# Performance work log

Measured on AMD Instinct MI355X. Metric: run time of the kernel, lower is better.

Reference implementation:

```python
import jax, jax.numpy as jnp
import numpy as np

NUM_USER = 10000
NUM_ITEM = 30000
N = NUM_USER + NUM_ITEM          # total nodes
DIM = 64                          # dim_E == dim_C
E = 500000                        # user-item interactions
NUM_ROUTING = 3
ALPHA_THR = 0.5
NEG_SLOPE_ATTN = 0.2              # GAT attention leaky slope
NEG_SLOPE_ACT = 0.01              # F.leaky_relu_ default


def l2norm(x, eps=1e-12):
    n = jnp.linalg.norm(x, axis=-1, keepdims=True)
    return x / jnp.maximum(n, eps)


def seg_softmax(score, seg):
    # numerically-stable softmax over edges grouped by destination node
    m = jax.ops.segment_max(score, seg, num_segments=N)
    e = jnp.exp(score - m[seg])
    s = jax.ops.segment_sum(e, seg, num_segments=N)
    return e / (s[seg] + 1e-16)


def gat_ori(x, W, src, dst):
    # GATConv_ori: dot-product attention, softmax per destination, scatter-add
    h = x @ W                                     # [N, C]
    score = jax.nn.leaky_relu(jnp.sum(h[dst] * h[src], -1), NEG_SLOPE_ATTN)
    alpha = seg_softmax(score, dst)               # [2E]
    return jax.ops.segment_sum(alpha[:, None] * h[src], dst, num_segments=N)


def gat_pre(x, y, z, W, src, dst):
    # GATConv_pre: primary-modality attention modulated by cross-modal gate (reattn)
    hx = x @ W
    sx = jnp.sum(hx[dst] * hx[src], -1)
    sy = jnp.sum(y[dst] * y[src], -1)
    sz = jnp.sum(z[dst] * z[src], -1)
    alpha = seg_softmax(jax.nn.leaky_relu(sx, NEG_SLOPE_ATTN), dst)
    gate = jax.nn.sigmoid(0.5 * (sy + sz))
    alpha = jnp.where(gate > ALPHA_THR, alpha * gate, alpha)
    return jax.ops.segment_sum(alpha[:, None] * hx[src], dst, num_segments=N)


def cgcn(pref, feat, pref2, feat2, pref3, feat3, src, dst, Wpre, Wori):
    x = jnp.concatenate([pref, feat], 0)
    y = jnp.concatenate([pref2, feat2], 0)
    z = jnp.concatenate([pref3, feat3], 0)
    x = l2norm(gat_pre(x, y, z, Wpre, src, dst))
    for _ in range(NUM_ROUTING):
        x = l2norm(x + gat_ori(x, Wori, src, dst))
    return x


def gcn_conv(x, W, src, dst):
    return jax.ops.segment_sum((x @ W)[src], dst, num_segments=N)


def real_gcn(id_emb, Wg, src, dst):
    x = l2norm(id_emb)
    h1 = jax.nn.leaky_relu(gcn_conv(x, Wg[0], src, dst), NEG_SLOPE_ACT)
    h2 = jax.nn.leaky_relu(gcn_conv(h1, Wg[1], src, dst), NEG_SLOPE_ACT)
    h3 = gcn_conv(h1, Wg[2], src, dst)
    return x + h1 + h2 + h3


def setup_inputs() -> dict:
    key = jax.random.key(0)
    ks = jax.random.split(key, 16)
    users = jax.random.randint(ks[0], (E,), 0, NUM_USER)
    items = jax.random.randint(ks[1], (E,), NUM_USER, N)
    edge_index = jnp.stack([users, items]).astype(jnp.int64)
    s = 0.05
    return {
        'edge_index': edge_index,
        'v_feat': jax.random.normal(ks[2], (NUM_ITEM, 128), jnp.float32),
        'a_feat': jax.random.normal(ks[3], (NUM_ITEM, 128), jnp.float32),
        't_feat': jax.random.normal(ks[4], (NUM_ITEM, 100), jnp.float32),
        'pref_v': jax.random.normal(ks[5], (NUM_USER, DIM), jnp.float32) * s,
        'pref_a': jax.random.normal(ks[6], (NUM_USER, DIM), jnp.float32) * s,
        'pref_t': jax.random.normal(ks[7], (NUM_USER, DIM), jnp.float32) * s,
        'mlp_v_w': jax.random.normal(ks[8], (DIM, 128), jnp.float32) * s,
        'mlp_v_b': jnp.zeros((DIM,), jnp.float32),
        'mlp_a_w': jax.random.normal(ks[9], (DIM, 128), jnp.float32) * s,
        'mlp_a_b': jnp.zeros((DIM,), jnp.float32),
        'mlp_t_w': jax.random.normal(ks[10], (DIM, 100), jnp.float32) * s,
        'mlp_t_b': jnp.zeros((DIM,), jnp.float32),
        'pre_w': jax.random.normal(ks[11], (3, DIM, DIM), jnp.float32) * s,
        'ori_w': jax.random.normal(ks[12], (3, DIM, DIM), jnp.float32) * s,
        'gcn_w': jax.random.normal(ks[13], (3, DIM, DIM), jnp.float32) * s,
        'id_embedding': jax.random.normal(ks[14], (N, DIM), jnp.float32) * s,
    }


def reference(edge_index, v_feat, a_feat, t_feat, pref_v, pref_a, pref_t,
              mlp_v_w, mlp_v_b, mlp_a_w, mlp_a_b, mlp_t_w, mlp_t_b,
              pre_w, ori_w, gcn_w, id_embedding):
    # symmetrize edges (cat with flipped); no self-loops possible (bipartite)
    src = jnp.concatenate([edge_index[0], edge_index[1]])
    dst = jnp.concatenate([edge_index[1], edge_index[0]])

    fv = l2norm(jax.nn.leaky_relu(v_feat @ mlp_v_w.T + mlp_v_b, NEG_SLOPE_ACT))
    fa = l2norm(jax.nn.leaky_relu(a_feat @ mlp_a_w.T + mlp_a_b, NEG_SLOPE_ACT))
    ft = l2norm(jax.nn.leaky_relu(t_feat @ mlp_t_w.T + mlp_t_b, NEG_SLOPE_ACT))
    pv, pa, pt = l2norm(pref_v), l2norm(pref_a), l2norm(pref_t)

    v_rep = cgcn(pv, fv, pa, fa, pt, ft, src, dst, pre_w[0], ori_w[0])
    a_rep = cgcn(pa, fa, pv, fv, pt, ft, src, dst, pre_w[1], ori_w[1])
    t_rep = cgcn(pt, ft, pa, fa, pv, fv, src, dst, pre_w[2], ori_w[2])
    id_rep = real_gcn(id_embedding, gcn_w, src, dst)

    return jnp.concatenate([id_rep, v_rep, a_rep, t_rep], axis=1)  # [N, 4*DIM]
```

## Files before the change

kernel.cpp:

```cpp
#include <hip/hip_runtime.h>
#include <hip/hip_fp16.h>
#include <math.h>

#define NUSER 10000
#define NITEM 30000
#define NN    40000
#define DD    64
#define PLANE ((size_t)NN * DD)

typedef _Float16 hv2 __attribute__((ext_vector_type(2)));
typedef _Float16 half8v __attribute__((ext_vector_type(8)));
typedef float float4v __attribute__((ext_vector_type(4)));
union U2H { unsigned u; hv2 v; __half2 hh; };

#if defined(__has_builtin)
#if __has_builtin(__builtin_amdgcn_fdot2)
#define HAS_FDOT2 1
#endif
#endif

__device__ __forceinline__ float fdot2u(unsigned a, unsigned b, float c) {
#ifdef HAS_FDOT2
    U2H x, y;
    x.u = a;
    y.u = b;
    return __builtin_amdgcn_fdot2(x.v, y.v, c, false);
#else
    U2H x, y;
    x.u = a;
    y.u = b;
    float2 fa = __half22float2(x.hh), fb = __half22float2(y.hh);
    return c + fa.x * fb.x + fa.y * fb.y;
#endif
}

__device__ __forceinline__ float dot8(uint4 a, uint4 b) {
    float d = fdot2u(a.x, b.x, 0.f);
    d = fdot2u(a.y, b.y, d);
    d = fdot2u(a.z, b.z, d);
    d = fdot2u(a.w, b.w, d);
    return d;
}

__device__ __forceinline__ __half2 uh(unsigned u) { U2H x; x.u = u; return x.hh; }
__device__ __forceinline__ unsigned hu(__half2 h) { U2H x; x.hh = h; return x.u; }
__device__ __forceinline__ __half2 h2rx(__half2 v, int m) {
    return __hadd2(v, uh((unsigned)__shfl_xor((int)hu(v), m, 64)));
}

__device__ __forceinline__ float wsum(float v) {
#pragma unroll
    for (int o = 32; o > 0; o >>= 1) v += __shfl_xor(v, o, 64);
    return v;
}
__device__ __forceinline__ float qsum8(float v) {
    v += __shfl_xor(v, 1, 64);
    v += __shfl_xor(v, 2, 64);
    v += __shfl_xor(v, 4, 64);
    return v;
}
__device__ __forceinline__ float gsum8(float v) {
    v += __shfl_xor(v, 8, 64);
    v += __shfl_xor(v, 16, 64);
    v += __shfl_xor(v, 32, 64);
    return v;
}

__device__ __forceinline__ int nodeperm(int i) {
    return ((i & 3) == 0) ? (i >> 2) : (NUSER + i - 1 - (i >> 2));
}

__global__ void k_hist(const int* ei, int E2, int E, int* cnt, int* posw) {
    int i = blockIdx.x * blockDim.x + threadIdx.x;
    if (i >= E2) return;
    int d = (i < E) ? ei[E + i] : ei[i - E];
    posw[i] = atomicAdd(&cnt[d], 1);
}

__global__ void k_bsum(const int* __restrict__ cnt, int* __restrict__ bsum, int n, int chunk) {
    __shared__ int wsh[4];
    int b = blockIdx.x, tid = threadIdx.x;
    int base = b * chunk, end = min(n, base + chunk);
    int s = 0;
    for (int i = base + tid; i < end; i += 256) s += cnt[i];
#pragma unroll
    for (int o = 32; o > 0; o >>= 1) s += __shfl_xor(s, o, 64);
    if ((tid & 63) == 0) wsh[tid >> 6] = s;
    __syncthreads();
    if (tid == 0) bsum[b] = wsh[0] + wsh[1] + wsh[2] + wsh[3];
}

__global__ void k_bscan(int* bsum, int nb, int* rp_end) {
    int lane = threadIdx.x;
    int v = (lane < nb) ? bsum[lane] : 0;
    int orig = v;
#pragma unroll
    for (int o = 1; o < 64; o <<= 1) {
        int y = __shfl_up(v, o, 64);
        if (lane >= o) v += y;
    }
    if (lane < nb) bsum[lane] = v - orig;
    if (lane == 63) *rp_end = v;
}

__global__ void k_apply(const int* __restrict__ cnt, const int* __restrict__ boff,
                        int* __restrict__ rp, int n, int chunk) {
    __shared__ int buf[256];
    __shared__ int csh;
    int b = blockIdx.x, tid = threadIdx.x;
    int base = b * chunk, end = min(n, base + chunk);
    int carry = boff[b];
    for (int t0 = base; t0 < end; t0 += 256) {
        int i = t0 + tid;
        int v = (i < end) ? cnt[i] : 0;
        int x = v;
        buf[tid] = x;
        __syncthreads();
        for (int o = 1; o < 256; o <<= 1) {
            int y = (tid >= o) ? buf[tid - o] : 0;
            __syncthreads();
            x += y;
            buf[tid] = x;
            __syncthreads();
        }
        if (i < end) rp[i] = carry + x - v;
        __syncthreads();
        if (tid == 255) csh = carry + x;
        __syncthreads();
        carry = csh;
    }
}

__global__ void k_scatter(const int* ei, int E2, int E, const int* rp,
                          const int* __restrict__ posw, int* col) {
    int i = blockIdx.x * blockDim.x + threadIdx.x;
    if (i >= E2) return;
    int j = (i < E) ? i : i - E;
    int s = (i < E) ? ei[j] : ei[E + j];
    int d = (i < E) ? ei[E + j] : ei[j];
    col[rp[d] + posw[i]] = s;
}

__global__ void k_prep_pref(const float* __restrict__ pv, const float* __restrict__ pa,
                            const float* __restrict__ pt, __half* __restrict__ M) {
    int t = blockIdx.x * blockDim.x + threadIdx.x;
    int w = t >> 6, lane = t & 63, nw = (gridDim.x * blockDim.x) >> 6;
    for (int r = w; r < NUSER; r += nw) {
        float a = pv[(size_t)r * DD + lane];
        float b = pa[(size_t)r * DD + lane];
        float c = pt[(size_t)r * DD + lane];
        float sa = a * a, sb = b * b, sc = c * c;
#pragma unroll
        for (int o = 32; o > 0; o >>= 1) {
            sa += __shfl_xor(sa, o, 64);
            sb += __shfl_xor(sb, o, 64);
            sc += __shfl_xor(sc, o, 64);
        }
        size_t base = (size_t)r * 3 * DD + lane;
        M[base] = __float2half(a / fmaxf(sqrtf(sa), 1e-12f));
        M[base + DD] = __float2half(b / fmaxf(sqrtf(sb), 1e-12f));
        M[base + 2 * DD] = __float2half(c / fmaxf(sqrtf(sc), 1e-12f));
    }
}

template <int K>
__global__ void k_mlp(const float* __restrict__ feat, const float* __restrict__ W,
                      const float* __restrict__ bias, __half* __restrict__ M, int mo) {
    constexpr int K4 = K / 4;
    __shared__ float4 Wl[K4][DD];
    __shared__ float4 rbuf[4][2][K4];
    int t = threadIdx.x, wib = t >> 6, lane = t & 63;
    for (int i = t; i < DD * K4; i += 256) {
        int c = i / K4, k4 = i - c * K4;
        Wl[k4][c] = *(const float4*)(W + (size_t)c * K + k4 * 4);
    }
    __syncthreads();
    float b = bias[lane];
    const int stride = gridDim.x * 4;
    int r = blockIdx.x * 4 + wib;
    float4 v = {0.f, 0.f, 0.f, 0.f};
    if (r < NITEM && lane < K4) v = *(const float4*)(feat + (size_t)r * K + lane * 4);
    int cur = 0;
    for (; r < NITEM; r += stride) {
        if (lane < K4) rbuf[wib][cur][lane] = v;
        int rn = r + stride;
        if (rn < NITEM && lane < K4) v = *(const float4*)(feat + (size_t)rn * K + lane * 4);
        asm volatile("s_waitcnt lgkmcnt(0)" ::: "memory");
        float acc = b;
#pragma unroll
        for (int k4 = 0; k4 < K4; k4++) {
            float4 x4 = rbuf[wib][cur][k4];
            float4 w4 = Wl[k4][lane];
            acc += x4.x * w4.x + x4.y * w4.y + x4.z * w4.z + x4.w * w4.w;
        }
        float h = acc > 0.f ? acc : 0.01f * acc;
        float n = sqrtf(wsum(h * h));
        M[((size_t)(NUSER + r) * 3 + mo) * DD + lane] = __float2half(h / fmaxf(n, 1e-12f));
        cur ^= 1;
    }
}

__global__ void k_gemm_mfma(const __half* __restrict__ x3, const float* __restrict__ W3,
                            __half* __restrict__ o3) {
    int mo = blockIdx.y;
    const float* W = W3 + (size_t)mo * 4096;
    int t = threadIdx.x, wv = t >> 6, lane = t & 63;
    int lr = lane & 15, lg = lane >> 4;
    half8v b[4][2];
#pragma unroll
    for (int ct = 0; ct < 4; ct++)
#pragma unroll
        for (int kh = 0; kh < 2; kh++)
#pragma unroll
            for (int i = 0; i < 8; i++)
                b[ct][kh][i] = (_Float16)W[(kh * 32 + lg * 8 + i) * 64 + ct * 16 + lr];
    const int NT = NN / 16;
    for (int rt = blockIdx.x * 4 + wv; rt < NT; rt += gridDim.x * 4) {
        const __half* xr = x3 + ((size_t)(rt * 16 + lr) * 3 + mo) * DD + lg * 8;
        half8v a0 = *(const half8v*)xr;
        half8v a1 = *(const half8v*)(xr + 32);
        float4v acc0 = {0.f, 0.f, 0.f, 0.f}, acc1 = acc0, acc2 = acc0, acc3 = acc0;
        acc0 = __builtin_amdgcn_mfma_f32_16x16x32_f16(a0, b[0][0], acc0, 0, 0, 0);
        acc1 = __builtin_amdgcn_mfma_f32_16x16x32_f16(a0, b[1][0], acc1, 0, 0, 0);
        acc2 = __builtin_amdgcn_mfma_f32_16x16x32_f16(a0, b[2][0], acc2, 0, 0, 0);
        acc3 = __builtin_amdgcn_mfma_f32_16x16x32_f16(a0, b[3][0], acc3, 0, 0, 0);
        acc0 = __builtin_amdgcn_mfma_f32_16x16x32_f16(a1, b[0][1], acc0, 0, 0, 0);
        acc1 = __builtin_amdgcn_mfma_f32_16x16x32_f16(a1, b[1][1], acc1, 0, 0, 0);
        acc2 = __builtin_amdgcn_mfma_f32_16x16x32_f16(a1, b[2][1], acc2, 0, 0, 0);
        acc3 = __builtin_amdgcn_mfma_f32_16x16x32_f16(a1, b[3][1], acc3, 0, 0, 0);
#pragma unroll
        for (int i = 0; i < 4; i++) {
            size_t rbase = ((size_t)(rt * 16 + lg * 4 + i) * 3 + mo) * DD + lr;
            o3[rbase] = __float2half(acc0[i]);
            o3[rbase + 16] = __float2half(acc1[i]);
            o3[rbase + 32] = __float2half(acc2[i]);
            o3[rbase + 48] = __float2half(acc3[i]);
        }
    }
}

__global__ void k_gemm_f2(const float* __restrict__ x, const float* __restrict__ W2,
                          __half* __restrict__ o2) {
    __shared__ float rowbuf[4][DD];
    int mo = blockIdx.y;
    const float* W = W2 + (size_t)mo * 4096;
    int t = threadIdx.x, wib = t >> 6, lane = t & 63;
    float Wc[DD];
#pragma unroll
    for (int k = 0; k < DD; k++) Wc[k] = W[k * DD + lane];
    for (int r = blockIdx.x * 4 + wib; r < NN; r += gridDim.x * 4) {
        rowbuf[wib][lane] = x[(size_t)r * DD + lane];
        asm volatile("s_waitcnt lgkmcnt(0)" ::: "memory");
        float acc = 0.f;
#pragma unroll
        for (int k4 = 0; k4 < DD / 4; k4++) {
            float4 xq = *(const float4*)&rowbuf[wib][k4 * 4];
            acc += xq.x * Wc[k4 * 4] + xq.y * Wc[k4 * 4 + 1] + xq.z * Wc[k4 * 4 + 2] +
                   xq.w * Wc[k4 * 4 + 3];
        }
        o2[((size_t)r * 2 + mo) * DD + lane] = __float2half(acc);
    }
}

__global__ void k_gemm_id(const float* __restrict__ x, const float* __restrict__ W,
                          __half* __restrict__ hout, float* __restrict__ xnorm) {
    __shared__ float rowbuf[4][DD];
    int t = threadIdx.x, wib = t >> 6, lane = t & 63;
    float Wc[DD];
#pragma unroll
    for (int k = 0; k < DD; k++) Wc[k] = W[k * DD + lane];
    for (int r = blockIdx.x * 4 + wib; r < NN; r += gridDim.x * 4) {
        float xv = x[(size_t)r * DD + lane];
        float n = sqrtf(wsum(xv * xv));
        xv /= fmaxf(n, 1e-12f);
        xnorm[(size_t)r * DD + lane] = xv;
        rowbuf[wib][lane] = xv;
        asm volatile("s_waitcnt lgkmcnt(0)" ::: "memory");
        float acc = 0.f;
#pragma unroll
        for (int k4 = 0; k4 < DD / 4; k4++) {
            float4 xq = *(const float4*)&rowbuf[wib][k4 * 4];
            acc += xq.x * Wc[k4 * 4] + xq.y * Wc[k4 * 4 + 1] + xq.z * Wc[k4 * 4 + 2] +
                   xq.w * Wc[k4 * 4 + 3];
        }
        hout[(size_t)r * DD + lane] = __float2half(acc);
    }
}

__device__ __forceinline__ float gatef(float ssum) {
    float gate = 1.f / (1.f + __expf(-0.5f * ssum));
    return gate > 0.5f ? gate : 1.f;
}

__global__ void k_edgedot3(const __half* __restrict__ M, const int* __restrict__ rp,
                           const int* __restrict__ col, __half* __restrict__ gf4) {
    int t = blockIdx.x * blockDim.x + threadIdx.x;
    int wv = t >> 6, lane = t & 63, nw = (gridDim.x * blockDim.x) >> 6;
    int g = lane >> 3, q = lane & 7;
    for (int w0 = wv; w0 < NN; w0 += nw) {
        int n = nodeperm(w0);
        int e0 = rp[n], e1 = rp[n + 1];
        if (e0 == e1) continue;
        const uint4* trow = (const uint4*)(M + (size_t)n * 192);
        uint4 tv = trow[q], ta = trow[q + 8], tt = trow[q + 16];
        for (int eb = e0 + g; eb < e1; eb += 8) {
            int sn = col[eb];
            const uint4* srow = (const uint4*)(M + (size_t)sn * 192);
            uint4 sv = srow[q], sa = srow[q + 8], st = srow[q + 16];
            float dv = dot8(tv, sv), da = dot8(ta, sa), dt = dot8(tt, st);
            dv = qsum8(dv);
            da = qsum8(da);
            dt = qsum8(dt);
            if (q == 0) {
                U2H p01, p2;
                p01.hh = __floats2half2_rn(gatef(da + dt), gatef(dv + dt));
                p2.hh = __floats2half2_rn(gatef(da + dv), 0.f);
                *(uint2*)(gf4 + (size_t)eb * 4) = make_uint2(p01.u, p2.u);
            }
        }
    }
}

__global__ void k_gat_pre3(const __half* __restrict__ h3, const __half* __restrict__ gf4,
                           const int* __restrict__ rp, const int* __restrict__ col,
                           __half* __restrict__ x3h) {
    int t = blockIdx.x * blockDim.x + threadIdx.x;
    int wv = t >> 6, lane = t & 63, nw = (gridDim.x * blockDim.x) >> 6;
    int g = lane >> 3, q = lane & 7;
    const __half2 z = __floats2half2_rn(0.f, 0.f);
    for (int w0 = wv; w0 < NN; w0 += nw) {
        int n = nodeperm(w0);
        int e0 = rp[n], e1 = rp[n + 1];
        const uint4* hrow = (const uint4*)(h3 + (size_t)n * 192);
        uint4 hd0 = hrow[q], hd1 = hrow[q + 8], hd2 = hrow[q + 16];
        float s0 = 0.f, s1 = 0.f, s2 = 0.f;
        __half2 a0[4] = {z, z, z, z}, a1[4] = {z, z, z, z}, a2[4] = {z, z, z, z};
        for (int eb = e0 + g; eb < e1; eb += 8) {
            int sn = col[eb];
            const uint4* srow = (const uint4*)(h3 + (size_t)sn * 192);
            uint4 v0 = srow[q], v1 = srow[q + 8], v2 = srow[q + 16];
            uint2 gv = *(const uint2*)(gf4 + (size_t)eb * 4);
            float d0 = dot8(hd0, v0), d1 = dot8(hd1, v1), d2 = dot8(hd2, v2);
            d0 = qsum8(d0);
            d1 = qsum8(d1);
            d2 = qsum8(d2);
            float2 g01 = __half22float2(uh(gv.x));
            float g2 = __half22float2(uh(gv.y)).x;
            float sc0 = d0 > 0.f ? d0 : 0.2f * d0;
            float sc1 = d1 > 0.f ? d1 : 0.2f * d1;
            float sc2 = d2 > 0.f ? d2 : 0.2f * d2;
            float p0 = __expf(sc0), p1 = __expf(sc1), p2 = __expf(sc2);
            s0 += p0;
            s1 += p1;
            s2 += p2;
            __half2 ph0 = __float2half2_rn(p0 * g01.x);
            __half2 ph1 = __float2half2_rn(p1 * g01.y);
            __half2 ph2 = __float2half2_rn(p2 * g2);
            a0[0] = __hfma2(ph0, uh(v0.x), a0[0]);
            a0[1] = __hfma2(ph0, uh(v0.y), a0[1]);
            a0[2] = __hfma2(ph0, uh(v0.z), a0[2]);
            a0[3] = __hfma2(ph0, uh(v0.w), a0[3]);
            a1[0] = __hfma2(ph1, uh(v1.x), a1[0]);
            a1[1] = __hfma2(ph1, uh(v1.y), a1[1]);
            a1[2] = __hfma2(ph1, uh(v1.z), a1[2]);
            a1[3] = __hfma2(ph1, uh(v1.w), a1[3]);
            a2[0] = __hfma2(ph2, uh(v2.x), a2[0]);
            a2[1] = __hfma2(ph2, uh(v2.y), a2[1]);
            a2[2] = __hfma2(ph2, uh(v2.z), a2[2]);
            a2[3] = __hfma2(ph2, uh(v2.w), a2[3]);
        }
        s0 = gsum8(s0);
        s1 = gsum8(s1);
        s2 = gsum8(s2);
#pragma unroll
        for (int j = 0; j < 4; j++) {
            a0[j] = h2rx(h2rx(h2rx(a0[j], 8), 16), 32);
            a1[j] = h2rx(h2rx(h2rx(a1[j], 8), 16), 32);
            a2[j] = h2rx(h2rx(h2rx(a2[j], 8), 16), 32);
        }
        float i0 = 1.f / (s0 + 1e-16f), i1 = 1.f / (s1 + 1e-16f), i2 = 1.f / (s2 + 1e-16f);
        float o0[8], o1[8], o2[8];
#pragma unroll
        for (int j = 0; j < 4; j++) {
            float2 f0 = __half22float2(a0[j]);
            float2 f1 = __half22float2(a1[j]);
            float2 f2 = __half22float2(a2[j]);
            o0[2 * j] = f0.x * i0;
            o0[2 * j + 1] = f0.y * i0;
            o1[2 * j] = f1.x * i1;
            o1[2 * j + 1] = f1.y * i1;
            o2[2 * j] = f2.x * i2;
            o2[2 * j + 1] = f2.y * i2;
        }
        float n0 = 0.f, n1 = 0.f, n2 = 0.f;
#pragma unroll
        for (int k = 0; k < 8; k++) {
            n0 += o0[k] * o0[k];
            n1 += o1[k] * o1[k];
            n2 += o2[k] * o2[k];
        }
        n0 = qsum8(n0);
        n1 = qsum8(n1);
        n2 = qsum8(n2);
        float r0 = 1.f / fmaxf(sqrtf(n0), 1e-12f);
        float r1 = 1.f / fmaxf(sqrtf(n1), 1e-12f);
        float r2 = 1.f / fmaxf(sqrtf(n2), 1e-12f);
        if (g == 0) {
            uint4* orow = (uint4*)(x3h + (size_t)n * 192);
            uint4 w0_, w1_, w2_;
            w0_.x = hu(__floats2half2_rn(o0[0] * r0, o0[1] * r0));
            w0_.y = hu(__floats2half2_rn(o0[2] * r0, o0[3] * r0));
            w0_.z = hu(__floats2half2_rn(o0[4] * r0, o0[5] * r0));
            w0_.w = hu(__floats2half2_rn(o0[6] * r0, o0[7] * r0));
            w1_.x = hu(__floats2half2_rn(o1[0] * r1, o1[1] * r1));
            w1_.y = hu(__floats2half2_rn(o1[2] * r1, o1[3] * r1));
            w1_.z = hu(__floats2half2_rn(o1[4] * r1, o1[5] * r1));
            w1_.w = hu(__floats2half2_rn(o1[6] * r1, o1[7] * r1));
            w2_.x = hu(__floats2half2_rn(o2[0] * r2, o2[1] * r2));
            w2_.y = hu(__floats2half2_rn(o2[2] * r2, o2[3] * r2));
            w2_.z = hu(__floats2half2_rn(o2[4] * r2, o2[5] * r2));
            w2_.w = hu(__floats2half2_rn(o2[6] * r2, o2[7] * r2));
            orow[q] = w0_;
            orow[q + 8] = w1_;
            orow[q + 16] = w2_;
        }
    }
}

__global__ void k_gat_ori3(const __half* __restrict__ h3, const __half* __restrict__ x3h,
                           const int* __restrict__ rp, const int* __restrict__ col,
                           __half* __restrict__ xout, float* __restrict__ fout) {
    int t = blockIdx.x * blockDim.x + threadIdx.x;
    int wv = t >> 6, lane = t & 63, nw = (gridDim.x * blockDim.x) >> 6;
    int g = lane >> 3, q = lane & 7;
    const __half2 z = __floats2half2_rn(0.f, 0.f);
    for (int w0 = wv; w0 < NN; w0 += nw) {
        int n = nodeperm(w0);
        int e0 = rp[n], e1 = rp[n + 1];
        const uint4* hrow = (const uint4*)(h3 + (size_t)n * 192);
        uint4 hd0 = hrow[q], hd1 = hrow[q + 8], hd2 = hrow[q + 16];
        float s0 = 0.f, s1 = 0.f, s2 = 0.f;
        __half2 a0[4] = {z, z, z, z}, a1[4] = {z, z, z, z}, a2[4] = {z, z, z, z};
        for (int eb = e0 + g; eb < e1; eb += 8) {
            int sn = col[eb];
            const uint4* srow = (const uint4*)(h3 + (size_t)sn * 192);
            uint4 v0 = srow[q], v1 = srow[q + 8], v2 = srow[q + 16];
            float d0 = dot8(hd0, v0), d1 = dot8(hd1, v1), d2 = dot8(hd2, v2);
            d0 = qsum8(d0);
            d1 = qsum8(d1);
            d2 = qsum8(d2);
            float sc0 = d0 > 0.f ? d0 : 0.2f * d0;
            float sc1 = d1 > 0.f ? d1 : 0.2f * d1;
            float sc2 = d2 > 0.f ? d2 : 0.2f * d2;
            float p0 = __expf(sc0), p1 = __expf(sc1), p2 = __expf(sc2);
            s0 += p0;
            s1 += p1;
            s2 += p2;
            __half2 ph0 = __float2half2_rn(p0);
            __half2 ph1 = __float2half2_rn(p1);
            __half2 ph2 = __float2half2_rn(p2);
            a0[0] = __hfma2(ph0, uh(v0.x), a0[0]);
            a0[1] = __hfma2(ph0, uh(v0.y), a0[1]);
            a0[2] = __hfma2(ph0, uh(v0.z), a0[2]);
            a0[3] = __hfma2(ph0, uh(v0.w), a0[3]);
            a1[0] = __hfma2(ph1, uh(v1.x), a1[0]);
            a1[1] = __hfma2(ph1, uh(v1.y), a1[1]);
            a1[2] = __hfma2(ph1, uh(v1.z), a1[2]);
            a1[3] = __hfma2(ph1, uh(v1.w), a1[3]);
            a2[0] = __hfma2(ph2, uh(v2.x), a2[0]);
            a2[1] = __hfma2(ph2, uh(v2.y), a2[1]);
            a2[2] = __hfma2(ph2, uh(v2.z), a2[2]);
            a2[3] = __hfma2(ph2, uh(v2.w), a2[3]);
        }
        s0 = gsum8(s0);
        s1 = gsum8(s1);
        s2 = gsum8(s2);
#pragma unroll
        for (int j = 0; j < 4; j++) {
            a0[j] = h2rx(h2rx(h2rx(a0[j], 8), 16), 32);
            a1[j] = h2rx(h2rx(h2rx(a1[j], 8), 16), 32);
            a2[j] = h2rx(h2rx(h2rx(a2[j], 8), 16), 32);
        }
        float i0 = 1.f / (s0 + 1e-16f), i1 = 1.f / (s1 + 1e-16f), i2 = 1.f / (s2 + 1e-16f);
        const uint4* xrow = (const uint4*)(x3h + (size_t)n * 192);
        uint4 xr0 = xrow[q], xr1 = xrow[q + 8], xr2 = xrow[q + 16];
        float o0[8], o1[8], o2[8];
#pragma unroll
        for (int j = 0; j < 4; j++) {
            float2 f0 = __half22float2(a0[j]);
            float2 f1 = __half22float2(a1[j]);
            float2 f2 = __half22float2(a2[j]);
            float2 xf0 = __half22float2(uh(j == 0 ? xr0.x : j == 1 ? xr0.y : j == 2 ? xr0.z : xr0.w));
            float2 xf1 = __half22float2(uh(j == 0 ? xr1.x : j == 1 ? xr1.y : j == 2 ? xr1.z : xr1.w));
            float2 xf2 = __half22float2(uh(j == 0 ? xr2.x : j == 1 ? xr2.y : j == 2 ? xr2.z : xr2.w));
            o0[2 * j] = xf0.x + f0.x * i0;
            o0[2 * j + 1] = xf0.y + f0.y * i0;
            o1[2 * j] = xf1.x + f1.x * i1;
            o1[2 * j + 1] = xf1.y + f1.y * i1;
            o2[2 * j] = xf2.x + f2.x * i2;
            o2[2 * j + 1] = xf2.y + f2.y * i2;
        }
        float n0 = 0.f, n1 = 0.f, n2 = 0.f;
#pragma unroll
        for (int k = 0; k < 8; k++) {
            n0 += o0[k] * o0[k];
            n1 += o1[k] * o1[k];
            n2 += o2[k] * o2[k];
        }
        n0 = qsum8(n0);
        n1 = qsum8(n1);
        n2 = qsum8(n2);
        float r0 = 1.f / fmaxf(sqrtf(n0), 1e-12f);
        float r1 = 1.f / fmaxf(sqrtf(n1), 1e-12f);
        float r2 = 1.f / fmaxf(sqrtf(n2), 1e-12f);
        if (g == 0) {
            if (fout) {
                float* ob = fout + (size_t)n * 256 + 64 + q * 8;
                float4 wa, wb;
                wa = make_float4(o0[0] * r0, o0[1] * r0, o0[2] * r0, o0[3] * r0);
                wb = make_float4(o0[4] * r0, o0[5] * r0, o0[6] * r0, o0[7] * r0);
                *(float4*)(ob) = wa;
                *(float4*)(ob + 4) = wb;
                wa = make_float4(o1[0] * r1, o1[1] * r1, o1[2] * r1, o1[3] * r1);
                wb = make_float4(o1[4] * r1, o1[5] * r1, o1[6] * r1, o1[7] * r1);
                *(float4*)(ob + 64) = wa;
                *(float4*)(ob + 68) = wb;
                wa = make_float4(o2[0] * r2, o2[1] * r2, o2[2] * r2, o2[3] * r2);
                wb = make_float4(o2[4] * r2, o2[5] * r2, o2[6] * r2, o2[7] * r2);
                *(float4*)(ob + 128) = wa;
                *(float4*)(ob + 132) = wb;
            } else {
                uint4* orow = (uint4*)(xout + (size_t)n * 192);
                uint4 w0_, w1_, w2_;
                w0_.x = hu(__floats2half2_rn(o0[0] * r0, o0[1] * r0));
                w0_.y = hu(__floats2half2_rn(o0[2] * r0, o0[3] * r0));
                w0_.z = hu(__floats2half2_rn(o0[4] * r0, o0[5] * r0));
                w0_.w = hu(__floats2half2_rn(o0[6] * r0, o0[7] * r0));
                w1_.x = hu(__floats2half2_rn(o1[0] * r1, o1[1] * r1));
                w1_.y = hu(__floats2half2_rn(o1[2] * r1, o1[3] * r1));
                w1_.z = hu(__floats2half2_rn(o1[4] * r1, o1[5] * r1));
                w1_.w = hu(__floats2half2_rn(o1[6] * r1, o1[7] * r1));
                w2_.x = hu(__floats2half2_rn(o2[0] * r2, o2[1] * r2));
                w2_.y = hu(__floats2half2_rn(o2[2] * r2, o2[3] * r2));
                w2_.z = hu(__floats2half2_rn(o2[4] * r2, o2[5] * r2));
                w2_.w = hu(__floats2half2_rn(o2[6] * r2, o2[7] * r2));
                orow[q] = w0_;
                orow[q + 8] = w1_;
                orow[q + 16] = w2_;
            }
        }
    }
}

__global__ void k_gcn1(const __half* __restrict__ h, const int* __restrict__ rp,
                       const int* __restrict__ col, float* __restrict__ out) {
    int t = blockIdx.x * blockDim.x + threadIdx.x;
    int wv = t >> 6, lane = t & 63, nw = (gridDim.x * blockDim.x) >> 6;
    int g = lane >> 3, q = lane & 7;
    const __half2 z = __floats2half2_rn(0.f, 0.f);
    for (int w0 = wv; w0 < NN; w0 += nw) {
        int n = nodeperm(w0);
        int e0 = rp[n], e1 = rp[n + 1];
        __half2 a[4] = {z, z, z, z};
        for (int eb = e0 + g; eb < e1; eb += 8) {
            int sn = col[eb];
            uint4 v = ((const uint4*)(h + (size_t)sn * DD))[q];
            a[0] = __hadd2(a[0], uh(v.x));
            a[1] = __hadd2(a[1], uh(v.y));
            a[2] = __hadd2(a[2], uh(v.z));
            a[3] = __hadd2(a[3], uh(v.w));
        }
#pragma unroll
        for (int j = 0; j < 4; j++) a[j] = h2rx(h2rx(h2rx(a[j], 8), 16), 32);
        if (g == 0) {
            float o[8];
#pragma unroll
            for (int j = 0; j < 4; j++) {
                float2 f = __half22float2(a[j]);
                o[2 * j] = f.x > 0.f ? f.x : 0.01f * f.x;
                o[2 * j + 1] = f.y > 0.f ? f.y : 0.01f * f.y;
            }
            float* ob = out + (size_t)n * DD + q * 8;
            *(float4*)(ob) = make_float4(o[0], o[1], o[2], o[3]);
            *(float4*)(ob + 4) = make_float4(o[4], o[5], o[6], o[7]);
        }
    }
}

__global__ void k_gcn_final2(const __half* __restrict__ gp, const int* __restrict__ rp,
                             const int* __restrict__ col, const float* __restrict__ x0,
                             const float* __restrict__ h1, float* __restrict__ out) {
    int t = blockIdx.x * blockDim.x + threadIdx.x;
    int wv = t >> 6, lane = t & 63, nw = (gridDim.x * blockDim.x) >> 6;
    int g = lane >> 3, q = lane & 7;
    const __half2 z = __floats2half2_rn(0.f, 0.f);
    for (int w0 = wv; w0 < NN; w0 += nw) {
        int n = nodeperm(w0);
        int e0 = rp[n], e1 = rp[n + 1];
        __half2 aA[4] = {z, z, z, z}, aB[4] = {z, z, z, z};
        for (int eb = e0 + g; eb < e1; eb += 8) {
            int sn = col[eb];
            const uint4* base = (const uint4*)(gp + (size_t)sn * 128);
            uint4 vA = base[q], vB = base[q + 8];
            aA[0] = __hadd2(aA[0], uh(vA.x));
            aA[1] = __hadd2(aA[1], uh(vA.y));
            aA[2] = __hadd2(aA[2], uh(vA.z));
            aA[3] = __hadd2(aA[3], uh(vA.w));
            aB[0] = __hadd2(aB[0], uh(vB.x));
            aB[1] = __hadd2(aB[1], uh(vB.y));
            aB[2] = __hadd2(aB[2], uh(vB.z));
            aB[3] = __hadd2(aB[3], uh(vB.w));
        }
#pragma unroll
        for (int j = 0; j < 4; j++) {
            aA[j] = h2rx(h2rx(h2rx(aA[j], 8), 16), 32);
            aB[j] = h2rx(h2rx(h2rx(aB[j], 8), 16), 32);
        }
        if (g == 0) {
            const float* p0 = x0 + (size_t)n * DD + q * 8;
            const float* p1 = h1 + (size_t)n * DD + q * 8;
            float4 v0a = *(const float4*)(p0), v0b = *(const float4*)(p0 + 4);
            float4 v1a = *(const float4*)(p1), v1b = *(const float4*)(p1 + 4);
            float o[8];
#pragma unroll
            for (int j = 0; j < 4; j++) {
                float2 fA = __half22float2(aA[j]);
                float2 fB = __half22float2(aB[j]);
                float h2x = fA.x > 0.f ? fA.x : 0.01f * fA.x;
                float h2y = fA.y > 0.f ? fA.y : 0.01f * fA.y;
                o[2 * j] = h2x + fB.x;
                o[2 * j + 1] = h2y + fB.y;
            }
            float* ob = out + (size_t)n * 256 + q * 8;
            *(float4*)(ob) = make_float4(o[0] + v0a.x + v1a.x, o[1] + v0a.y + v1a.y,
                                         o[2] + v0a.z + v1a.z, o[3] + v0a.w + v1a.w);
            *(float4*)(ob + 4) = make_float4(o[4] + v0b.x + v1b.x, o[5] + v0b.y + v1b.y,
                                             o[6] + v0b.z + v1b.z, o[7] + v0b.w + v1b.w);
        }
    }
}

extern "C" void kernel_launch(void* const* d_in, const int* in_sizes, int n_in,
                              void* d_out, int out_size, void* d_ws, size_t ws_size,
                              hipStream_t stream) {
    const int* ei       = (const int*)d_in[0];
    const float* v_feat = (const float*)d_in[1];
    const float* a_feat = (const float*)d_in[2];
    const float* t_feat = (const float*)d_in[3];
    const float* pref_v = (const float*)d_in[4];
    const float* pref_a = (const float*)d_in[5];
    const float* pref_t = (const float*)d_in[6];
    const float* mlp_v_w = (const float*)d_in[7];
    const float* mlp_v_b = (const float*)d_in[8];
    const float* mlp_a_w = (const float*)d_in[9];
    const float* mlp_a_b = (const float*)d_in[10];
    const float* mlp_t_w = (const float*)d_in[11];
    const float* mlp_t_b = (const float*)d_in[12];
    const float* pre_w  = (const float*)d_in[13];
    const float* ori_w  = (const float*)d_in[14];
    const float* gcn_w  = (const float*)d_in[15];
    const float* id_emb = (const float*)d_in[16];
    float* out = (float*)d_out;

    const int E2 = in_sizes[0];
    const int E  = E2 / 2;

    char* w = (char*)d_ws;
    auto alloc = [&](size_t bytes) -> void* {
        void* p = (void*)w;
        w += (bytes + 255) & ~(size_t)255;
        return p;
    };
    int* cnt  = (int*)alloc((size_t)NN * 4);
    int* rp   = (int*)alloc((size_t)(NN + 1) * 4);
    int* bsum = (int*)alloc(256);
    int* col  = (int*)alloc((size_t)E2 * 4);
    int* posw = (int*)alloc((size_t)E2 * 4);
    __half* Mh3  = (__half*)alloc(3 * PLANE * 2);
    __half* hb3h = (__half*)alloc(3 * PLANE * 2);
    __half* x3h  = (__half*)alloc(3 * PLANE * 2);
    __half* gf4  = (__half*)alloc((size_t)E2 * 4 * 2);
    float* x0f = (float*)alloc(PLANE * 4);
    float* h1f = (float*)alloc(PLANE * 4);

    __half* g1 = hb3h;
    __half* gpair = hb3h + PLANE;

    const int NBLK = 64, CHUNK = (NN + NBLK - 1) / NBLK;
    hipMemsetAsync(cnt, 0, (size_t)NN * 4, stream);
    k_hist<<<(E2 + 255) / 256, 256, 0, stream>>>(ei, E2, E, cnt, posw);
    k_bsum<<<NBLK, 256, 0, stream>>>(cnt, bsum, NN, CHUNK);
    k_bscan<<<1, 64, 0, stream>>>(bsum, NBLK, rp + NN);
    k_apply<<<NBLK, 256, 0, stream>>>(cnt, bsum, rp, NN, CHUNK);
    k_scatter<<<(E2 + 255) / 256, 256, 0, stream>>>(ei, E2, E, rp, posw, col);

    k_prep_pref<<<640, 256, 0, stream>>>(pref_v, pref_a, pref_t, Mh3);
    k_mlp<128><<<1024, 256, 0, stream>>>(v_feat, mlp_v_w, mlp_v_b, Mh3, 0);
    k_mlp<128><<<1024, 256, 0, stream>>>(a_feat, mlp_a_w, mlp_a_b, Mh3, 1);
    k_mlp<100><<<1024, 256, 0, stream>>>(t_feat, mlp_t_w, mlp_t_b, Mh3, 2);

    const int GB = (NN + 3) / 4;

    k_edgedot3<<<GB, 256, 0, stream>>>(Mh3, rp, col, gf4);

    dim3 gm(640, 3);
    k_gemm_mfma<<<gm, 256, 0, stream>>>(Mh3, pre_w, hb3h);
    k_gat_pre3<<<GB, 256, 0, stream>>>(hb3h, gf4, rp, col, x3h);
    for (int it = 0; it < 3; it++) {
        k_gemm_mfma<<<gm, 256, 0, stream>>>(x3h, ori_w, hb3h);
        if (it < 2)
            k_gat_ori3<<<GB, 256, 0, stream>>>(hb3h, x3h, rp, col, x3h, nullptr);
        else
            k_gat_ori3<<<GB, 256, 0, stream>>>(hb3h, x3h, rp, col, nullptr, out);
    }

    k_gemm_id<<<1280, 256, 0, stream>>>(id_emb, gcn_w, g1, x0f);
    k_gcn1<<<GB, 256, 0, stream>>>(g1, rp, col, h1f);
    dim3 g2(1280, 2);
    k_gemm_f2<<<g2, 256, 0, stream>>>(h1f, gcn_w + 4096, gpair);
    k_gcn_final2<<<GB, 256, 0, stream>>>(gpair, rp, col, x0f, h1f, out);
}
```

Baseline: 554.2 us.

## Map eight destination nodes per wavefront instead of one node per wave

All edge-aggregation kernels now give each 8-lane group its own destination node and walk that node's edges serially, instead of spreading one node's edges across the eight groups of a wave. This drops the cross-group shuffle reductions and the single-group writeback, and it shrinks the grid by eight. The node ordering now interleaves users and items in blocks of eight. The cost is load imbalance inside a wave when degrees differ, and longer serial edge loops per lane group.

```diff
diff --git a/kernel.cpp b/kernel.cpp
--- a/kernel.cpp
+++ b/kernel.cpp
@@ -44,9 +44,6 @@
 
 __device__ __forceinline__ __half2 uh(unsigned u) { U2H x; x.u = u; return x.hh; }
 __device__ __forceinline__ unsigned hu(__half2 h) { U2H x; x.hh = h; return x.u; }
-__device__ __forceinline__ __half2 h2rx(__half2 v, int m) {
-    return __hadd2(v, uh((unsigned)__shfl_xor((int)hu(v), m, 64)));
-}
 
 __device__ __forceinline__ float wsum(float v) {
 #pragma unroll
@@ -59,15 +56,9 @@
     v += __shfl_xor(v, 4, 64);
     return v;
 }
-__device__ __forceinline__ float gsum8(float v) {
-    v += __shfl_xor(v, 8, 64);
-    v += __shfl_xor(v, 16, 64);
-    v += __shfl_xor(v, 32, 64);
-    return v;
-}
-
-__device__ __forceinline__ int nodeperm(int i) {
-    return ((i & 3) == 0) ? (i >> 2) : (NUSER + i - 1 - (i >> 2));
+
+__device__ __forceinline__ int unitbase(int u) {
+    return ((u & 3) == 0) ? ((u >> 2) * 8) : (NUSER + (u - (u >> 2) - 1) * 8);
 }
 
 __global__ void k_hist(const int* ei, int E2, int E, int* cnt, int* posw) {
@@ -297,25 +288,23 @@
     int t = blockIdx.x * blockDim.x + threadIdx.x;
     int wv = t >> 6, lane = t & 63, nw = (gridDim.x * blockDim.x) >> 6;
     int g = lane >> 3, q = lane & 7;
-    for (int w0 = wv; w0 < NN; w0 += nw) {
-        int n = nodeperm(w0);
+    for (int u = wv; u < NN / 8; u += nw) {
+        int n = unitbase(u) + g;
         int e0 = rp[n], e1 = rp[n + 1];
-        if (e0 == e1) continue;
         const uint4* trow = (const uint4*)(M + (size_t)n * 192);
         uint4 tv = trow[q], ta = trow[q + 8], tt = trow[q + 16];
-        for (int eb = e0 + g; eb < e1; eb += 8) {
-            int sn = col[eb];
+        for (int e = e0; e < e1; e++) {
+            int sn = col[e];
             const uint4* srow = (const uint4*)(M + (size_t)sn * 192);
             uint4 sv = srow[q], sa = srow[q + 8], st = srow[q + 16];
-            float dv = dot8(tv, sv), da = dot8(ta, sa), dt = dot8(tt, st);
-            dv = qsum8(dv);
-            da = qsum8(da);
-            dt = qsum8(dt);
+            float dv = qsum8(dot8(tv, sv));
+            float da = qsum8(dot8(ta, sa));
+            float dt = qsum8(dot8(tt, st));
             if (q == 0) {
                 U2H p01, p2;
                 p01.hh = __floats2half2_rn(gatef(da + dt), gatef(dv + dt));
                 p2.hh = __floats2half2_rn(gatef(da + dv), 0.f);
-                *(uint2*)(gf4 + (size_t)eb * 4) = make_uint2(p01.u, p2.u);
+                *(uint2*)(gf4 + (size_t)e * 4) = make_uint2(p01.u, p2.u);
             }
         }
     }
@@ -328,22 +317,21 @@
     int wv = t >> 6, lane = t & 63, nw = (gridDim.x * blockDim.x) >> 6;
     int g = lane >> 3, q = lane & 7;
     const __half2 z = __floats2half2_rn(0.f, 0.f);
-    for (int w0 = wv; w0 < NN; w0 += nw) {
-        int n = nodeperm(w0);
+    for (int u = wv; u < NN / 8; u += nw) {
+        int n = unitbase(u) + g;
         int e0 = rp[n], e1 = rp[n + 1];
         const uint4* hrow = (const uint4*)(h3 + (size_t)n * 192);
         uint4 hd0 = hrow[q], hd1 = hrow[q + 8], hd2 = hrow[q + 16];
         float s0 = 0.f, s1 = 0.f, s2 = 0.f;
         __half2 a0[4] = {z, z, z, z}, a1[4] = {z, z, z, z}, a2[4] = {z, z, z, z};
-        for (int eb = e0 + g; eb < e1; eb += 8) {
-            int sn = col[eb];
+        for (int e = e0; e < e1; e++) {
+            int sn = col[e];
             const uint4* srow = (const uint4*)(h3 + (size_t)sn * 192);
             uint4 v0 = srow[q], v1 = srow[q + 8], v2 = srow[q + 16];
-            uint2 gv = *(const uint2*)(gf4 + (size_t)eb * 4);
-            float d0 = dot8(hd0, v0), d1 = dot8(hd1, v1), d2 = dot8(hd2, v2);
-            d0 = qsum8(d0);
-            d1 = qsum8(d1);
-            d2 = qsum8(d2);
+            uint2 gv = *(const uint2*)(gf4 + (size_t)e * 4);
+            float d0 = qsum8(dot8(hd0, v0));
+            float d1 = qsum8(dot8(hd1, v1));
+            float d2 = qsum8(dot8(hd2, v2));
             float2 g01 = __half22float2(uh(gv.x));
             float g2 = __half22float2(uh(gv.y)).x;
             float sc0 = d0 > 0.f ? d0 : 0.2f * d0;
@@ -369,15 +357,6 @@
             a2[2] = __hfma2(ph2, uh(v2.z), a2[2]);
             a2[3] = __hfma2(ph2, uh(v2.w), a2[3]);
         }
-        s0 = gsum8(s0);
-        s1 = gsum8(s1);
-        s2 = gsum8(s2);
-#pragma unroll
-        for (int j = 0; j < 4; j++) {
-            a0[j] = h2rx(h2rx(h2rx(a0[j], 8), 16), 32);
-            a1[j] = h2rx(h2rx(h2rx(a1[j], 8), 16), 32);
-            a2[j] = h2rx(h2rx(h2rx(a2[j], 8), 16), 32);
-        }
         float i0 = 1.f / (s0 + 1e-16f), i1 = 1.f / (s1 + 1e-16f), i2 = 1.f / (s2 + 1e-16f);
         float o0[8], o1[8], o2[8];
 #pragma unroll
@@ -405,25 +384,23 @@
         float r0 = 1.f / fmaxf(sqrtf(n0), 1e-12f);
         float r1 = 1.f / fmaxf(sqrtf(n1), 1e-12f);
         float r2 = 1.f / fmaxf(sqrtf(n2), 1e-12f);
-        if (g == 0) {
-            uint4* orow = (uint4*)(x3h + (size_t)n * 192);
-            uint4 w0_, w1_, w2_;
-            w0_.x = hu(__floats2half2_rn(o0[0] * r0, o0[1] * r0));
-            w0_.y = hu(__floats2half2_rn(o0[2] * r0, o0[3] * r0));
-            w0_.z = hu(__floats2half2_rn(o0[4] * r0, o0[5] * r0));
-            w0_.w = hu(__floats2half2_rn(o0[6] * r0, o0[7] * r0));
-            w1_.x = hu(__floats2half2_rn(o1[0] * r1, o1[1] * r1));
-            w1_.y = hu(__floats2half2_rn(o1[2] * r1, o1[3] * r1));
-            w1_.z = hu(__floats2half2_rn(o1[4] * r1, o1[5] * r1));
-            w1_.w = hu(__floats2half2_rn(o1[6] * r1, o1[7] * r1));
-            w2_.x = hu(__floats2half2_rn(o2[0] * r2, o2[1] * r2));
-            w2_.y = hu(__floats2half2_rn(o2[2] * r2, o2[3] * r2));
-            w2_.z = hu(__floats2half2_rn(o2[4] * r2, o2[5] * r2));
-            w2_.w = hu(__floats2half2_rn(o2[6] * r2, o2[7] * r2));
-            orow[q] = w0_;
-            orow[q + 8] = w1_;
-            orow[q + 16] = w2_;
-        }
+        uint4* orow = (uint4*)(x3h + (size_t)n * 192);
+        uint4 w0_, w1_, w2_;
+        w0_.x = hu(__floats2half2_rn(o0[0] * r0, o0[1] * r0));
+        w0_.y = hu(__floats2half2_rn(o0[2] * r0, o0[3] * r0));
+        w0_.z = hu(__floats2half2_rn(o0[4] * r0, o0[5] * r0));
+        w0_.w = hu(__floats2half2_rn(o0[6] * r0, o0[7] * r0));
+        w1_.x = hu(__floats2half2_rn(o1[0] * r1, o1[1] * r1));
+        w1_.y = hu(__floats2half2_rn(o1[2] * r1, o1[3] * r1));
+        w1_.z = hu(__floats2half2_rn(o1[4] * r1, o1[5] * r1));
+        w1_.w = hu(__floats2half2_rn(o1[6] * r1, o1[7] * r1));
+        w2_.x = hu(__floats2half2_rn(o2[0] * r2, o2[1] * r2));
+        w2_.y = hu(__floats2half2_rn(o2[2] * r2, o2[3] * r2));
+        w2_.z = hu(__floats2half2_rn(o2[4] * r2, o2[5] * r2));
+        w2_.w = hu(__floats2half2_rn(o2[6] * r2, o2[7] * r2));
+        orow[q] = w0_;
+        orow[q + 8] = w1_;
+        orow[q + 16] = w2_;
     }
 }
 
@@ -434,21 +411,20 @@
     int wv = t >> 6, lane = t & 63, nw = (gridDim.x * blockDim.x) >> 6;
     int g = lane >> 3, q = lane & 7;
     const __half2 z = __floats2half2_rn(0.f, 0.f);
-    for (int w0 = wv; w0 < NN; w0 += nw) {
-        int n = nodeperm(w0);
+    for (int u = wv; u < NN / 8; u += nw) {
+        int n = unitbase(u) + g;
         int e0 = rp[n], e1 = rp[n + 1];
         const uint4* hrow = (const uint4*)(h3 + (size_t)n * 192);
         uint4 hd0 = hrow[q], hd1 = hrow[q + 8], hd2 = hrow[q + 16];
         float s0 = 0.f, s1 = 0.f, s2 = 0.f;
         __half2 a0[4] = {z, z, z, z}, a1[4] = {z, z, z, z}, a2[4] = {z, z, z, z};
-        for (int eb = e0 + g; eb < e1; eb += 8) {
-            int sn = col[eb];
+        for (int e = e0; e < e1; e++) {
+            int sn = col[e];
             const uint4* srow = (const uint4*)(h3 + (size_t)sn * 192);
             uint4 v0 = srow[q], v1 = srow[q + 8], v2 = srow[q + 16];
-            float d0 = dot8(hd0, v0), d1 = dot8(hd1, v1), d2 = dot8(hd2, v2);
-            d0 = qsum8(d0);
-            d1 = qsum8(d1);
-            d2 = qsum8(d2);
+            float d0 = qsum8(dot8(hd0, v0));
+            float d1 = qsum8(dot8(hd1, v1));
+            float d2 = qsum8(dot8(hd2, v2));
             float sc0 = d0 > 0.f ? d0 : 0.2f * d0;
             float sc1 = d1 > 0.f ? d1 : 0.2f * d1;
             float sc2 = d2 > 0.f ? d2 : 0.2f * d2;
@@ -472,15 +448,6 @@
             a2[2] = __hfma2(ph2, uh(v2.z), a2[2]);
             a2[3] = __hfma2(ph2, uh(v2.w), a2[3]);
         }
-        s0 = gsum8(s0);
-        s1 = gsum8(s1);
-        s2 = gsum8(s2);
-#pragma unroll
-        for (int j = 0; j < 4; j++) {
-            a0[j] = h2rx(h2rx(h2rx(a0[j], 8), 16), 32);
-            a1[j] = h2rx(h2rx(h2rx(a1[j], 8), 16), 32);
-            a2[j] = h2rx(h2rx(h2rx(a2[j], 8), 16), 32);
-        }
         float i0 = 1.f / (s0 + 1e-16f), i1 = 1.f / (s1 + 1e-16f), i2 = 1.f / (s2 + 1e-16f);
         const uint4* xrow = (const uint4*)(x3h + (size_t)n * 192);
         uint4 xr0 = xrow[q], xr1 = xrow[q + 8], xr2 = xrow[q + 16];
@@ -513,41 +480,32 @@
         float r0 = 1.f / fmaxf(sqrtf(n0), 1e-12f);
         float r1 = 1.f / fmaxf(sqrtf(n1), 1e-12f);
         float r2 = 1.f / fmaxf(sqrtf(n2), 1e-12f);
-        if (g == 0) {
-            if (fout) {
-                float* ob = fout + (size_t)n * 256 + 64 + q * 8;
-                float4 wa, wb;
-                wa = make_float4(o0[0] * r0, o0[1] * r0, o0[2] * r0, o0[3] * r0);
-                wb = make_float4(o0[4] * r0, o0[5] * r0, o0[6] * r0, o0[7] * r0);
-                *(float4*)(ob) = wa;
-                *(float4*)(ob + 4) = wb;
-                wa = make_float4(o1[0] * r1, o1[1] * r1, o1[2] * r1, o1[3] * r1);
-                wb = make_float4(o1[4] * r1, o1[5] * r1, o1[6] * r1, o1[7] * r1);
-                *(float4*)(ob + 64) = wa;
-                *(float4*)(ob + 68) = wb;
-                wa = make_float4(o2[0] * r2, o2[1] * r2, o2[2] * r2, o2[3] * r2);
-                wb = make_float4(o2[4] * r2, o2[5] * r2, o2[6] * r2, o2[7] * r2);
-                *(float4*)(ob + 128) = wa;
-                *(float4*)(ob + 132) = wb;
-            } else {
-                uint4* orow = (uint4*)(xout + (size_t)n * 192);
-                uint4 w0_, w1_, w2_;
-                w0_.x = hu(__floats2half2_rn(o0[0] * r0, o0[1] * r0));
-                w0_.y = hu(__floats2half2_rn(o0[2] * r0, o0[3] * r0));
-                w0_.z = hu(__floats2half2_rn(o0[4] * r0, o0[5] * r0));
-                w0_.w = hu(__floats2half2_rn(o0[6] * r0, o0[7] * r0));
-                w1_.x = hu(__floats2half2_rn(o1[0] * r1, o1[1] * r1));
-                w1_.y = hu(__floats2half2_rn(o1[2] * r1, o1[3] * r1));
-                w1_.z = hu(__floats2half2_rn(o1[4] * r1, o1[5] * r1));
-                w1_.w = hu(__floats2half2_rn(o1[6] * r1, o1[7] * r1));
-                w2_.x = hu(__floats2half2_rn(o2[0] * r2, o2[1] * r2));
-                w2_.y = hu(__floats2half2_rn(o2[2] * r2, o2[3] * r2));
-                w2_.z = hu(__floats2half2_rn(o2[4] * r2, o2[5] * r2));
-                w2_.w = hu(__floats2half2_rn(o2[6] * r2, o2[7] * r2));
-                orow[q] = w0_;
-                orow[q + 8] = w1_;
-                orow[q + 16] = w2_;
-            }
+        if (fout) {
+            float* ob = fout + (size_t)n * 256 + 64 + q * 8;
+            *(float4*)(ob) = make_float4(o0[0] * r0, o0[1] * r0, o0[2] * r0, o0[3] * r0);
+            *(float4*)(ob + 4) = make_float4(o0[4] * r0, o0[5] * r0, o0[6] * r0, o0[7] * r0);
+            *(float4*)(ob + 64) = make_float4(o1[0] * r1, o1[1] * r1, o1[2] * r1, o1[3] * r1);
+            *(float4*)(ob + 68) = make_float4(o1[4] * r1, o1[5] * r1, o1[6] * r1, o1[7] * r1);
+            *(float4*)(ob + 128) = make_float4(o2[0] * r2, o2[1] * r2, o2[2] * r2, o2[3] * r2);
+            *(float4*)(ob + 132) = make_float4(o2[4] * r2, o2[5] * r2, o2[6] * r2, o2[7] * r2);
+        } else {
+            uint4* orow = (uint4*)(xout + (size_t)n * 192);
+            uint4 w0_, w1_, w2_;
+            w0_.x = hu(__floats2half2_rn(o0[0] * r0, o0[1] * r0));
+            w0_.y = hu(__floats2half2_rn(o0[2] * r0, o0[3] * r0));
+            w0_.z = hu(__floats2half2_rn(o0[4] * r0, o0[5] * r0));
+            w0_.w = hu(__floats2half2_rn(o0[6] * r0, o0[7] * r0));
+            w1_.x = hu(__floats2half2_rn(o1[0] * r1, o1[1] * r1));
+            w1_.y = hu(__floats2half2_rn(o1[2] * r1, o1[3] * r1));
+            w1_.z = hu(__floats2half2_rn(o1[4] * r1, o1[5] * r1));
+            w1_.w = hu(__floats2half2_rn(o1[6] * r1, o1[7] * r1));
+            w2_.x = hu(__floats2half2_rn(o2[0] * r2, o2[1] * r2));
+            w2_.y = hu(__floats2half2_rn(o2[2] * r2, o2[3] * r2));
+            w2_.z = hu(__floats2half2_rn(o2[4] * r2, o2[5] * r2));
+            w2_.w = hu(__floats2half2_rn(o2[6] * r2, o2[7] * r2));
+            orow[q] = w0_;
+            orow[q + 8] = w1_;
+            orow[q + 16] = w2_;
         }
     }
 }
@@ -558,32 +516,28 @@
     int wv = t >> 6, lane = t & 63, nw = (gridDim.x * blockDim.x) >> 6;
     int g = lane >> 3, q = lane & 7;
     const __half2 z = __floats2half2_rn(0.f, 0.f);
-    for (int w0 = wv; w0 < NN; w0 += nw) {
-        int n = nodeperm(w0);
+    for (int u = wv; u < NN / 8; u += nw) {
+        int n = unitbase(u) + g;
         int e0 = rp[n], e1 = rp[n + 1];
         __half2 a[4] = {z, z, z, z};
-        for (int eb = e0 + g; eb < e1; eb += 8) {
-            int sn = col[eb];
+        for (int e = e0; e < e1; e++) {
+            int sn = col[e];
             uint4 v = ((const uint4*)(h + (size_t)sn * DD))[q];
             a[0] = __hadd2(a[0], uh(v.x));
             a[1] = __hadd2(a[1], uh(v.y));
             a[2] = __hadd2(a[2], uh(v.z));
             a[3] = __hadd2(a[3], uh(v.w));
         }
-#pragma unroll
-        for (int j = 0; j < 4; j++) a[j] = h2rx(h2rx(h2rx(a[j], 8), 16), 32);
-        if (g == 0) {
-            float o[8];
-#pragma unroll
-            for (int j = 0; j < 4; j++) {
-                float2 f = __half22float2(a[j]);
-                o[2 * j] = f.x > 0.f ? f.x : 0.01f * f.x;
-                o[2 * j + 1] = f.y > 0.f ? f.y : 0.01f * f.y;
-            }
-            float* ob = out + (size_t)n * DD + q * 8;
-            *(float4*)(ob) = make_float4(o[0], o[1], o[2], o[3]);
-            *(float4*)(ob + 4) = make_float4(o[4], o[5], o[6], o[7]);
-        }
+        float o[8];
+#pragma unroll
+        for (int j = 0; j < 4; j++) {
+            float2 f = __half22float2(a[j]);
+            o[2 * j] = f.x > 0.f ? f.x : 0.01f * f.x;
+            o[2 * j + 1] = f.y > 0.f ? f.y : 0.01f * f.y;
+        }
+        float* ob = out + (size_t)n * DD + q * 8;
+        *(float4*)(ob) = make_float4(o[0], o[1], o[2], o[3]);
+        *(float4*)(ob + 4) = make_float4(o[4], o[5], o[6], o[7]);
     }
 }
 
@@ -594,12 +548,12 @@
     int wv = t >> 6, lane = t & 63, nw = (gridDim.x * blockDim.x) >> 6;
     int g = lane >> 3, q = lane & 7;
     const __half2 z = __floats2half2_rn(0.f, 0.f);
-    for (int w0 = wv; w0 < NN; w0 += nw) {
-        int n = nodeperm(w0);
+    for (int u = wv; u < NN / 8; u += nw) {
+        int n = unitbase(u) + g;
         int e0 = rp[n], e1 = rp[n + 1];
         __half2 aA[4] = {z, z, z, z}, aB[4] = {z, z, z, z};
-        for (int eb = e0 + g; eb < e1; eb += 8) {
-            int sn = col[eb];
+        for (int e = e0; e < e1; e++) {
+            int sn = col[e];
             const uint4* base = (const uint4*)(gp + (size_t)sn * 128);
             uint4 vA = base[q], vB = base[q + 8];
             aA[0] = __hadd2(aA[0], uh(vA.x));
@@ -611,32 +565,25 @@
             aB[2] = __hadd2(aB[2], uh(vB.z));
             aB[3] = __hadd2(aB[3], uh(vB.w));
         }
+        const float* p0 = x0 + (size_t)n * DD + q * 8;
+        const float* p1 = h1 + (size_t)n * DD + q * 8;
+        float4 v0a = *(const float4*)(p0), v0b = *(const float4*)(p0 + 4);
+        float4 v1a = *(const float4*)(p1), v1b = *(const float4*)(p1 + 4);
+        float o[8];
 #pragma unroll
         for (int j = 0; j < 4; j++) {
-            aA[j] = h2rx(h2rx(h2rx(aA[j], 8), 16), 32);
-            aB[j] = h2rx(h2rx(h2rx(aB[j], 8), 16), 32);
-        }
-        if (g == 0) {
-            const float* p0 = x0 + (size_t)n * DD + q * 8;
-            const float* p1 = h1 + (size_t)n * DD + q * 8;
-            float4 v0a = *(const float4*)(p0), v0b = *(const float4*)(p0 + 4);
-            float4 v1a = *(const float4*)(p1), v1b = *(const float4*)(p1 + 4);
-            float o[8];
-#pragma unroll
-            for (int j = 0; j < 4; j++) {
-                float2 fA = __half22float2(aA[j]);
-                float2 fB = __half22float2(aB[j]);
-                float h2x = fA.x > 0.f ? fA.x : 0.01f * fA.x;
-                float h2y = fA.y > 0.f ? fA.y : 0.01f * fA.y;
-                o[2 * j] = h2x + fB.x;
-                o[2 * j + 1] = h2y + fB.y;
-            }
-            float* ob = out + (size_t)n * 256 + q * 8;
-            *(float4*)(ob) = make_float4(o[0] + v0a.x + v1a.x, o[1] + v0a.y + v1a.y,
-                                         o[2] + v0a.z + v1a.z, o[3] + v0a.w + v1a.w);
-            *(float4*)(ob + 4) = make_float4(o[4] + v0b.x + v1b.x, o[5] + v0b.y + v1b.y,
-                                             o[6] + v0b.z + v1b.z, o[7] + v0b.w + v1b.w);
-        }
+            float2 fA = __half22float2(aA[j]);
+            float2 fB = __half22float2(aB[j]);
+            float h2x = fA.x > 0.f ? fA.x : 0.01f * fA.x;
+            float h2y = fA.y > 0.f ? fA.y : 0.01f * fA.y;
+            o[2 * j] = h2x + fB.x;
+            o[2 * j + 1] = h2y + fB.y;
+        }
+        float* ob = out + (size_t)n * 256 + q * 8;
+        *(float4*)(ob) = make_float4(o[0] + v0a.x + v1a.x, o[1] + v0a.y + v1a.y,
+                                     o[2] + v0a.z + v1a.z, o[3] + v0a.w + v1a.w);
+        *(float4*)(ob + 4) = make_float4(o[4] + v0b.x + v1b.x, o[5] + v0b.y + v1b.y,
+                                         o[6] + v0b.z + v1b.z, o[7] + v0b.w + v1b.w);
     }
 }
 
@@ -699,7 +646,7 @@
     k_mlp<128><<<1024, 256, 0, stream>>>(a_feat, mlp_a_w, mlp_a_b, Mh3, 1);
     k_mlp<100><<<1024, 256, 0, stream>>>(t_feat, mlp_t_w, mlp_t_b, Mh3, 2);
 
-    const int GB = (NN + 3) / 4;
+    const int GB = (NN / 8 + 3) / 4;
 
     k_edgedot3<<<GB, 256, 0, stream>>>(Mh3, rp, col, gf4);
 
```

After: 666.9 us. 1.2x slower.
